# Kernel optimization log

Hardware: AMD Instinct MI355X
Metric: run time of the kernel (lower is better)

Reference implementation:

```python
import jax, jax.numpy as jnp
import numpy as np

D = 256
FF = 1024
NH = 8
BZ, TL = 8, 1024
L, Hs, Ws = 1, 64, 64


def _linear(x, w, b):
    # torch nn.Linear convention: w is [out, in]
    return x @ w.T + b


def _ln(x, g, b, eps=1e-5):
    m = x.mean(-1, keepdims=True)
    v = ((x - m) ** 2).mean(-1, keepdims=True)
    return (x - m) / jnp.sqrt(v + eps) * g + b


def setup_inputs() -> dict:
    key = jax.random.key(0)
    ks = jax.random.split(key, 16)
    s = 0.02
    inp = {
        "tgt": jax.random.normal(ks[0], (BZ, TL, D), jnp.float32),
        "reference_points": jax.random.uniform(ks[1], (BZ, TL, 2), jnp.float32),
        "srcs": jax.random.normal(ks[2], (BZ, L, D, Hs, Ws), jnp.float32),
        "posemb_2d": jax.random.normal(ks[3], (BZ, TL, D), jnp.float32),
        # self-attn (nn.MultiheadAttention) params
        "in_proj_w": jax.random.normal(ks[4], (3 * D, D), jnp.float32) * s,
        "in_proj_b": jnp.zeros((3 * D,), jnp.float32),
        "out_proj_w": jax.random.normal(ks[5], (D, D), jnp.float32) * s,
        "out_proj_b": jnp.zeros((D,), jnp.float32),
        # hand-rolled cross-attn linears (q, k, v, out)
        "lin_q_w": jax.random.normal(ks[6], (D, D), jnp.float32) * s,
        "lin_q_b": jnp.zeros((D,), jnp.float32),
        "lin_k_w": jax.random.normal(ks[7], (D, D), jnp.float32) * s,
        "lin_k_b": jnp.zeros((D,), jnp.float32),
        "lin_v_w": jax.random.normal(ks[8], (D, D), jnp.float32) * s,
        "lin_v_b": jnp.zeros((D,), jnp.float32),
        "lin_o_w": jax.random.normal(ks[9], (D, D), jnp.float32) * s,
        "lin_o_b": jnp.zeros((D,), jnp.float32),
        # layer norms
        "norm1_g": jnp.ones((D,), jnp.float32),
        "norm1_b": jnp.zeros((D,), jnp.float32),
        "norm2_g": jnp.ones((D,), jnp.float32),
        "norm2_b": jnp.zeros((D,), jnp.float32),
        # FFN
        "ffn_w1": jax.random.normal(ks[10], (FF, D), jnp.float32) * s,
        "ffn_b1": jnp.zeros((FF,), jnp.float32),
        "ffn_w2": jax.random.normal(ks[11], (D, FF), jnp.float32) * s,
        "ffn_b2": jnp.zeros((D,), jnp.float32),
        "ffn_norm_g": jnp.ones((D,), jnp.float32),
        "ffn_norm_b": jnp.zeros((D,), jnp.float32),
    }
    return inp


def reference(tgt, reference_points, srcs, posemb_2d,
              in_proj_w, in_proj_b, out_proj_w, out_proj_b,
              lin_q_w, lin_q_b, lin_k_w, lin_k_b, lin_v_w, lin_v_b,
              lin_o_w, lin_o_b,
              norm1_g, norm1_b, norm2_g, norm2_b,
              ffn_w1, ffn_b1, ffn_w2, ffn_b2, ffn_norm_g, ffn_norm_b):
    bz, tl, c = tgt.shape
    nh = NH
    dh = c // nh
    scale = dh ** -0.5

    # ---- self-attention (nn.MultiheadAttention math) ----
    qk = tgt + posemb_2d  # q = k = with_pos_embed(tgt, posemb_2d_)
    wq, wk, wv = in_proj_w[:c], in_proj_w[c:2 * c], in_proj_w[2 * c:]
    bq, bk, bv = in_proj_b[:c], in_proj_b[c:2 * c], in_proj_b[2 * c:]
    qp = _linear(qk, wq, bq).reshape(bz, tl, nh, dh)
    kp = _linear(qk, wk, bk).reshape(bz, tl, nh, dh)
    vp = _linear(tgt, wv, bv).reshape(bz, tl, nh, dh)
    att = jax.nn.softmax(jnp.einsum('bqhd,bkhd->bhqk', qp * scale, kp), axis=-1)
    sa = jnp.einsum('bhqk,bkhd->bqhd', att, vp).reshape(bz, tl, c)
    sa = _linear(sa, out_proj_w, out_proj_b)
    tgt = _ln(tgt + sa, norm2_g, norm2_b)

    # ---- hand-rolled cross attention ----
    bz_, l, c_, h, w = srcs.shape
    s = jnp.transpose(srcs.reshape(bz_ * l, c_, h, w), (0, 2, 3, 1)).reshape(bz_ * l, h * w, c_)
    query = _linear(tgt, lin_q_w, lin_q_b)          # [bz, tl, c]
    key = _linear(s, lin_k_w, lin_k_b)              # [bz*l, hw, c]
    value = _linear(s, lin_v_w, lin_v_b)
    affinity = jax.nn.softmax(jnp.einsum('bqc,bkc->bqk', query, key), axis=-1)  # no 1/sqrt(d) scale, faithful
    tgt2 = _linear(jnp.einsum('bqk,bkc->bqc', affinity, value), lin_o_w, lin_o_b)
    tgt = _ln(tgt + tgt2, norm1_g, norm1_b)

    # ---- FFN ----
    src2 = _linear(jax.nn.relu(_linear(tgt, ffn_w1, ffn_b1)), ffn_w2, ffn_b2)
    tgt = _ln(tgt + src2, ffn_norm_g, ffn_norm_b)
    return tgt
```

## Files before the change

### kernel.cpp

```cpp
#include <hip/hip_runtime.h>
#include <hip/hip_bf16.h>
#include <math.h>

typedef __attribute__((ext_vector_type(8))) __bf16 bf16x8;
typedef __attribute__((ext_vector_type(4))) __bf16 bf16x4;
typedef __attribute__((ext_vector_type(2))) __bf16 bf16x2;
typedef __attribute__((ext_vector_type(4))) float  f32x4;

#define MFMA16(a,b,c) __builtin_amdgcn_mfma_f32_16x16x32_bf16((a),(b),(c),0,0,0)

__device__ __forceinline__ unsigned pack2bf(float a, float b){
  bf16x2 t; t[0] = (__bf16)a; t[1] = (__bf16)b;
  return __builtin_bit_cast(unsigned, t);
}
__device__ __forceinline__ int perm1(int r){ return ((r<<2)|(r>>1)) & 7; }

__device__ __forceinline__ bf16x8 cvt8(const float4& a, const float4& b){
  bf16x8 h;
  h[0]=(__bf16)a.x; h[1]=(__bf16)a.y; h[2]=(__bf16)a.z; h[3]=(__bf16)a.w;
  h[4]=(__bf16)b.x; h[5]=(__bf16)b.y; h[6]=(__bf16)b.z; h[7]=(__bf16)b.w;
  return h;
}

template<int BM, bool RELU, int OUTMODE, int AMODE>
__global__ __launch_bounds__(256) void gemm_bt(
    const void* __restrict__ Av, const float* __restrict__ A2,
    const float* __restrict__ W,
    const float* __restrict__ bias, void* __restrict__ Cv,
    int M, int N, int K, int ldc, int coff, float oscale)
{
  constexpr int MT = BM/32;
  constexpr int PASSES = BM/64;
  __shared__ __align__(16) __bf16 As[BM][72];
  __shared__ __align__(16) __bf16 Bs[64][72];

  const int tid  = threadIdx.x;
  const int wid  = tid >> 6;
  const int lane = tid & 63;
  const int wr   = wid >> 1;
  const int wc   = wid & 1;
  const int lq   = lane & 15;
  const int lk8  = (lane >> 4) << 3;
  const int rb   = (lane >> 4) << 2;

  const int m0 = blockIdx.x * BM;
  const int n0 = blockIdx.y * 64;

  const int sr = tid >> 2;
  const int sc = (tid & 3) << 4;

  f32x4 acc[MT][2];
  #pragma unroll
  for (int i=0;i<MT;i++)
    #pragma unroll
    for (int j=0;j<2;j++) acc[i][j] = f32x4{0.f,0.f,0.f,0.f};

  for (int k0=0; k0<K; k0+=64){
    __syncthreads();
    #pragma unroll
    for (int p=0;p<PASSES;p++){
      const int row = sr + p*64;
      if (AMODE == 2){
        const __bf16* ap = (const __bf16*)Av + (size_t)(m0+row)*K + k0 + sc;
        *(bf16x8*)&As[row][sc]   = *(const bf16x8*)(ap);
        *(bf16x8*)&As[row][sc+8] = *(const bf16x8*)(ap + 8);
      } else {
        const float* ap = (const float*)Av + (size_t)(m0+row)*K + k0 + sc;
        float4 a0 = *(const float4*)(ap);
        float4 a1 = *(const float4*)(ap+4);
        float4 a2 = *(const float4*)(ap+8);
        float4 a3 = *(const float4*)(ap+12);
        if (AMODE == 1){
          const float* bp = A2 + (size_t)(m0+row)*K + k0 + sc;
          const float4 b0 = *(const float4*)(bp);
          const float4 b1 = *(const float4*)(bp+4);
          const float4 b2 = *(const float4*)(bp+8);
          const float4 b3 = *(const float4*)(bp+12);
          a0.x+=b0.x; a0.y+=b0.y; a0.z+=b0.z; a0.w+=b0.w;
          a1.x+=b1.x; a1.y+=b1.y; a1.z+=b1.z; a1.w+=b1.w;
          a2.x+=b2.x; a2.y+=b2.y; a2.z+=b2.z; a2.w+=b2.w;
          a3.x+=b3.x; a3.y+=b3.y; a3.z+=b3.z; a3.w+=b3.w;
        }
        *(bf16x8*)&As[row][sc]   = cvt8(a0,a1);
        *(bf16x8*)&As[row][sc+8] = cvt8(a2,a3);
      }
    }
    {
      const float* wp = W + (size_t)(n0+sr)*K + k0 + sc;
      const float4 a0 = *(const float4*)(wp);
      const float4 a1 = *(const float4*)(wp+4);
      const float4 a2 = *(const float4*)(wp+8);
      const float4 a3 = *(const float4*)(wp+12);
      *(bf16x8*)&Bs[sr][sc]   = cvt8(a0,a1);
      *(bf16x8*)&Bs[sr][sc+8] = cvt8(a2,a3);
    }
    __syncthreads();
    #pragma unroll
    for (int ksub=0; ksub<2; ksub++){
      bf16x8 bfr[2];
      #pragma unroll
      for (int j=0;j<2;j++)
        bfr[j] = *(const bf16x8*)&Bs[wc*32 + j*16 + lq][ksub*32 + lk8];
      #pragma unroll
      for (int i=0;i<MT;i++){
        const bf16x8 af = *(const bf16x8*)&As[wr*(BM/2) + i*16 + lq][ksub*32 + lk8];
        acc[i][0] = MFMA16(af, bfr[0], acc[i][0]);
        acc[i][1] = MFMA16(af, bfr[1], acc[i][1]);
      }
    }
  }

  #pragma unroll
  for (int i=0;i<MT;i++)
    #pragma unroll
    for (int j=0;j<2;j++){
      const int coln = n0 + wc*32 + j*16 + lq;
      const float bv = bias ? bias[coln] : 0.f;
      if (OUTMODE == 2){
        const int rowm0 = m0 + wr*(BM/2) + i*16 + rb;
        bf16x4 hv;
        #pragma unroll
        for (int r=0;r<4;r++){
          float vv = (acc[i][j][r] + bv) * oscale;
          if (RELU) vv = fmaxf(vv, 0.f);
          hv[r] = (__bf16)vv;
        }
        *(bf16x4*)&((__bf16*)Cv)[((size_t)((rowm0>>10)*256) + coln)*1024 + (rowm0&1023)] = hv;
      } else {
        #pragma unroll
        for (int r=0;r<4;r++){
          const int rowm = m0 + wr*(BM/2) + i*16 + rb + r;
          float vv = (acc[i][j][r] + bv) * oscale;
          if (RELU) vv = fmaxf(vv, 0.f);
          const size_t idx = (size_t)rowm*ldc + coff + coln;
          if (OUTMODE == 1) ((__bf16*)Cv)[idx] = (__bf16)vv;
          else              ((float*)Cv)[idx]  = vv;
        }
      }
    }
}

__global__ __launch_bounds__(256) void gemm_srcs_kv(
    const float* __restrict__ S,
    const float* __restrict__ Wk, const float* __restrict__ bk,
    const float* __restrict__ Wv, const float* __restrict__ bv,
    __bf16* __restrict__ Kout, __bf16* __restrict__ Vt)
{
  extern __shared__ __bf16 lds[];
  __bf16* As = lds;
  __bf16* Bs = lds + 128*264;

  const int tid  = threadIdx.x;
  const int wid  = tid >> 6;
  const int lane = tid & 63;
  const int wr   = wid >> 1;
  const int wc   = wid & 1;
  const int lq   = lane & 15;
  const int lk8  = (lane >> 4) << 3;
  const int rb   = (lane >> 4) << 2;

  const int m0 = blockIdx.x * 128;
  const int bb = m0 >> 12;
  const int p0 = m0 & 4095;

  const int cA = tid & 31;
  const int qA = tid >> 5;
  for (int k0=0; k0<256; k0+=32){
    const float* sbase = &S[((size_t)bb*256 + k0 + cA)*4096 + p0];
    #pragma unroll
    for (int ps=0; ps<4; ps++){
      const int p = ps*32 + qA*4;
      const float4 f4 = *(const float4*)(sbase + p);
      As[(p+0)*264 + k0 + cA] = (__bf16)f4.x;
      As[(p+1)*264 + k0 + cA] = (__bf16)f4.y;
      As[(p+2)*264 + k0 + cA] = (__bf16)f4.z;
      As[(p+3)*264 + k0 + cA] = (__bf16)f4.w;
    }
  }

  const int sr  = tid >> 2;
  const int scb = (tid & 3) * 64;

  for (int half=0; half<2; half++){
    const float* W    = half ? Wv : Wk;
    const float* bias = half ? bv : bk;
    for (int nt=0; nt<4; nt++){
      const int n0 = nt*64;
      __syncthreads();
      {
        const float* wp = W + (size_t)(n0+sr)*256 + scb;
        #pragma unroll
        for (int j=0;j<4;j++){
          const float4 a0 = *(const float4*)(wp + j*16);
          const float4 a1 = *(const float4*)(wp + j*16 + 4);
          const float4 a2 = *(const float4*)(wp + j*16 + 8);
          const float4 a3 = *(const float4*)(wp + j*16 + 12);
          *(bf16x8*)&Bs[sr*264 + scb + j*16]     = cvt8(a0,a1);
          *(bf16x8*)&Bs[sr*264 + scb + j*16 + 8] = cvt8(a2,a3);
        }
      }
      __syncthreads();
      f32x4 acc[4][2];
      #pragma unroll
      for (int i=0;i<4;i++)
        #pragma unroll
        for (int j=0;j<2;j++) acc[i][j] = f32x4{0.f,0.f,0.f,0.f};
      #pragma unroll
      for (int k0=0; k0<256; k0+=32){
        bf16x8 bfr[2];
        #pragma unroll
        for (int j=0;j<2;j++)
          bfr[j] = *(const bf16x8*)&Bs[(wc*32 + j*16 + lq)*264 + k0 + lk8];
        #pragma unroll
        for (int i=0;i<4;i++){
          const bf16x8 af = *(const bf16x8*)&As[(wr*64 + i*16 + lq)*264 + k0 + lk8];
          acc[i][0] = MFMA16(af, bfr[0], acc[i][0]);
          acc[i][1] = MFMA16(af, bfr[1], acc[i][1]);
        }
      }
      #pragma unroll
      for (int i=0;i<4;i++)
        #pragma unroll
        for (int j=0;j<2;j++){
          const int coln = n0 + wc*32 + j*16 + lq;
          const float bvv = bias[coln];
          if (half){
            bf16x4 hv;
            #pragma unroll
            for (int r=0;r<4;r++) hv[r] = (__bf16)(acc[i][j][r] + bvv);
            *(bf16x4*)&Vt[((size_t)bb*256 + coln)*4096 + p0 + wr*64 + i*16 + rb] = hv;
          } else {
            #pragma unroll
            for (int r=0;r<4;r++){
              const int rowm = m0 + wr*64 + i*16 + rb + r;
              Kout[(size_t)rowm*256 + coln] = (__bf16)(acc[i][j][r] + bvv);
            }
          }
        }
    }
  }
}

__global__ __launch_bounds__(256) void ln_kernel(const float* __restrict__ res,
                                                 const float* __restrict__ x,
                                                 const float* __restrict__ g,
                                                 const float* __restrict__ beta,
                                                 float* __restrict__ out,
                                                 __bf16* __restrict__ outb)
{
  const int row  = blockIdx.x*4 + (threadIdx.x >> 6);
  const int lane = threadIdx.x & 63;
  const int c = lane*4;
  const float4 rv = *(const float4*)&res[(size_t)row*256 + c];
  const float4 xv = *(const float4*)&x[(size_t)row*256 + c];
  float v0=rv.x+xv.x, v1=rv.y+xv.y, v2=rv.z+xv.z, v3=rv.w+xv.w;
  float s = v0+v1+v2+v3;
  #pragma unroll
  for (int off=1; off<64; off<<=1) s += __shfl_xor(s, off);
  const float mean = s * (1.f/256.f);
  const float d0=v0-mean, d1=v1-mean, d2=v2-mean, d3=v3-mean;
  float q = d0*d0 + d1*d1 + d2*d2 + d3*d3;
  #pragma unroll
  for (int off=1; off<64; off<<=1) q += __shfl_xor(q, off);
  const float rstd = rsqrtf(q*(1.f/256.f) + 1e-5f);
  const float4 gv = *(const float4*)&g[c];
  const float4 bv = *(const float4*)&beta[c];
  float4 ov;
  ov.x = d0*rstd*gv.x + bv.x;
  ov.y = d1*rstd*gv.y + bv.y;
  ov.z = d2*rstd*gv.z + bv.z;
  ov.w = d3*rstd*gv.w + bv.w;
  *(float4*)&out[(size_t)row*256 + c] = ov;
  if (outb){
    bf16x4 hv;
    hv[0]=(__bf16)ov.x; hv[1]=(__bf16)ov.y; hv[2]=(__bf16)ov.z; hv[3]=(__bf16)ov.w;
    *(bf16x4*)&outb[(size_t)row*256 + c] = hv;
  }
}

__global__ __launch_bounds__(256) void flash_self(
    const __bf16* __restrict__ qks, const __bf16* __restrict__ vts,
    __bf16* __restrict__ sab)
{
  const int qt = blockIdx.x;
  const int b  = blockIdx.y >> 3;
  const int h  = blockIdx.y & 7;
  const int tid  = threadIdx.x;
  const int wid  = tid >> 6;
  const int lane = tid & 63;
  const int lq   = lane & 15;
  const int hi   = lane >> 4;
  const int lk8  = hi << 3;
  const int rb   = hi << 2;
  const float SCALE = 0.17677669529663687f;

  const int qrow = b*1024 + qt*64 + wid*16 + lq;
  const bf16x8 qf = *(const bf16x8*)&qks[(size_t)qrow*512 + h*32 + lk8];

  const __bf16* kb0 = &qks[(size_t)(b*1024 + lq)*512 + 256 + h*32 + lk8];
  const __bf16* vb0 = &vts[(size_t)(b*256 + h*32 + lq)*1024 + lk8];

  const f32x4 Z = {0.f, 0.f, 0.f, 0.f};
  float m = -1e30f, l = 0.f;
  f32x4 o0 = Z, o1 = Z;

  for (int it=0; it<16; ++it){
    const int key0 = it*64;
    f32x4 s4[4];
    #pragma unroll
    for (int kt=0;kt<4;kt++){
      const bf16x8 kf = *(const bf16x8*)(kb0 + (size_t)(key0 + kt*16)*512);
      s4[kt] = MFMA16(kf, qf, Z);
      #pragma unroll
      for (int r=0;r<4;r++) s4[kt][r] *= SCALE;
    }
    float pm = s4[0][0];
    #pragma unroll
    for (int kt=0;kt<4;kt++)
      #pragma unroll
      for (int r=0;r<4;r++) pm = fmaxf(pm, s4[kt][r]);
    pm = fmaxf(pm, __shfl_xor(pm,16));
    pm = fmaxf(pm, __shfl_xor(pm,32));
    if (!__all(pm <= m + 8.f)){
      const float mn = fmaxf(m, pm);
      const float alpha = __expf(m - mn);
      o0[0]*=alpha; o0[1]*=alpha; o0[2]*=alpha; o0[3]*=alpha;
      o1[0]*=alpha; o1[1]*=alpha; o1[2]*=alpha; o1[3]*=alpha;
      l *= alpha;
      m = mn;
    }
    float p[4][4]; float rs = 0.f;
    #pragma unroll
    for (int kt=0;kt<4;kt++)
      #pragma unroll
      for (int r=0;r<4;r++){ p[kt][r] = __expf(s4[kt][r]-m); rs += p[kt][r]; }
    rs += __shfl_xor(rs,16);
    rs += __shfl_xor(rs,32);
    l += rs;
    unsigned pk0[4], pk1[4];
    #pragma unroll
    for (int kt=0;kt<4;kt++){
      pk0[kt] = pack2bf(p[kt][0], p[kt][1]);
      pk1[kt] = pack2bf(p[kt][2], p[kt][3]);
    }
    const int srcA = ((hi&1)<<5) + lq;
    const int srcB = srcA + 16;
    const bool ksel = hi >= 2;
    bf16x8 pf[2];
    #pragma unroll
    for (int ks2=0; ks2<2; ks2++){
      const unsigned a0 = (unsigned)__shfl((int)pk0[2*ks2],   srcA);
      const unsigned a1 = (unsigned)__shfl((int)pk0[2*ks2+1], srcA);
      const unsigned b0 = (unsigned)__shfl((int)pk1[2*ks2],   srcA);
      const unsigned b1 = (unsigned)__shfl((int)pk1[2*ks2+1], srcA);
      const unsigned c0 = (unsigned)__shfl((int)pk0[2*ks2],   srcB);
      const unsigned c1 = (unsigned)__shfl((int)pk0[2*ks2+1], srcB);
      const unsigned d0 = (unsigned)__shfl((int)pk1[2*ks2],   srcB);
      const unsigned d1 = (unsigned)__shfl((int)pk1[2*ks2+1], srcB);
      union { unsigned u[4]; bf16x8 v; } uu;
      uu.u[0] = ksel ? a1 : a0;
      uu.u[1] = ksel ? b1 : b0;
      uu.u[2] = ksel ? c1 : c0;
      uu.u[3] = ksel ? d1 : d0;
      pf[ks2] = uu.v;
    }
    #pragma unroll
    for (int ks2=0; ks2<2; ks2++){
      const bf16x8 vf0 = *(const bf16x8*)(vb0 + key0 + ks2*32);
      const bf16x8 vf1 = *(const bf16x8*)(vb0 + (size_t)16*1024 + key0 + ks2*32);
      o0 = MFMA16(vf0, pf[ks2], o0);
      o1 = MFMA16(vf1, pf[ks2], o1);
    }
  }
  const float inv = 1.f / l;
  bf16x4 w0, w1;
  #pragma unroll
  for (int r=0;r<4;r++){ w0[r] = (__bf16)(o0[r]*inv); w1[r] = (__bf16)(o1[r]*inv); }
  *(bf16x4*)&sab[(size_t)qrow*256 + h*32 + rb]      = w0;
  *(bf16x4*)&sab[(size_t)qrow*256 + h*32 + 16 + rb] = w1;
}

__global__ __launch_bounds__(256, 1) void flash_cross(
    const __bf16* __restrict__ qgm, const __bf16* __restrict__ kg,
    const __bf16* __restrict__ vtg, __bf16* __restrict__ Opart,
    float* __restrict__ ml)
{
  extern __shared__ __bf16 smem[];
  __bf16* Ks = smem;
  __bf16* Vt = smem + 64*256;

  const int bid = blockIdx.x;
  const int xcd = bid & 7;
  const int grp = bid >> 3;
  const int qt  = grp & 7;
  const int pp  = xcd + 8*(grp >> 3);
  const int b   = pp >> 3;
  const int sl  = pp & 7;

  const int tid  = threadIdx.x;
  const int wid  = tid >> 6;
  const int lane = tid & 63;
  const int lq   = lane & 15;
  const int hi   = lane >> 4;
  const int lk8  = hi << 3;
  const int rb   = hi << 2;
  const int p1l  = perm1(lq & 7);

  const int q0 = b*1024 + qt*128 + wid*32;
  bf16x8 qf[2][8];
  #pragma unroll
  for (int g=0; g<2; g++)
    #pragma unroll
    for (int ks=0; ks<8; ks++)
      qf[g][ks] = *(const bf16x8*)&qgm[(size_t)(q0 + g*16 + lq)*256 + ks*32 + lk8];

  const f32x4 Z = {0.f, 0.f, 0.f, 0.f};
  float m[2] = {-1e30f, -1e30f};
  float l[2] = {0.f, 0.f};
  f32x4 o[2][16];
  #pragma unroll
  for (int g=0; g<2; g++)
    #pragma unroll
    for (int nf=0; nf<16; nf++) o[g][nf] = Z;

  const int srow = tid >> 2;
  const int c4   = tid & 3;
  const int p1s  = perm1(srow & 7);

  for (int it=0; it<8; ++it){
    const int key0 = sl*512 + it*64;
    __syncthreads();
    {
      const __bf16* kb = &kg[(size_t)(b*4096 + key0 + srow)*256];
      #pragma unroll
      for (int j=0;j<8;j++){
        const int ch = c4 + j*4;
        *(bf16x8*)&Ks[srow*256 + ((ch ^ p1s)<<3)] = *(const bf16x8*)(kb + ch*8);
      }
    }
    {
      #pragma unroll
      for (int ps=0; ps<4; ps++){
        const int d = srow + ps*64;
        const __bf16* vb = &vtg[(size_t)(b*256 + d)*4096 + key0];
        #pragma unroll
        for (int s2=0;s2<2;s2++){
          const int ch = c4 + s2*4;
          *(bf16x8*)&Vt[d*64 + ((ch ^ p1s)<<3)] = *(const bf16x8*)(vb + ch*8);
        }
      }
    }
    __syncthreads();
    f32x4 s4[2][4];
    #pragma unroll
    for (int g=0; g<2; g++)
      #pragma unroll
      for (int kt=0;kt<4;kt++) s4[g][kt] = Z;
    #pragma unroll
    for (int ks=0; ks<8; ks++){
      #pragma unroll
      for (int kt=0; kt<4; kt++){
        const bf16x8 kf = *(const bf16x8*)&Ks[(kt*16+lq)*256 + (((ks*4+hi) ^ p1l)<<3)];
        s4[0][kt] = MFMA16(kf, qf[0][ks], s4[0][kt]);
        s4[1][kt] = MFMA16(kf, qf[1][ks], s4[1][kt]);
      }
    }
    float pm[2];
    #pragma unroll
    for (int g=0; g<2; g++){
      float v = s4[g][0][0];
      #pragma unroll
      for (int kt=0;kt<4;kt++)
        #pragma unroll
        for (int r=0;r<4;r++) v = fmaxf(v, s4[g][kt][r]);
      v = fmaxf(v, __shfl_xor(v, 16));
      v = fmaxf(v, __shfl_xor(v, 32));
      pm[g] = v;
    }
    const bool need = (pm[0] > m[0] + 8.f) || (pm[1] > m[1] + 8.f);
    if (__any(need)){
      #pragma unroll
      for (int g=0; g<2; g++){
        const float mn = fmaxf(m[g], pm[g]);
        const float alpha = __expf(m[g] - mn);
        #pragma unroll
        for (int nf=0;nf<16;nf++){
          o[g][nf][0]*=alpha; o[g][nf][1]*=alpha;
          o[g][nf][2]*=alpha; o[g][nf][3]*=alpha;
        }
        l[g] *= alpha;
        m[g] = mn;
      }
    }
    bf16x8 pf[2][2];
    #pragma unroll
    for (int g=0; g<2; g++){
      float p[4][4];
      float rs = 0.f;
      #pragma unroll
      for (int kt=0;kt<4;kt++)
        #pragma unroll
        for (int r=0;r<4;r++){ p[kt][r] = __expf(s4[g][kt][r] - m[g]); rs += p[kt][r]; }
      rs += __shfl_xor(rs, 16);
      rs += __shfl_xor(rs, 32);
      l[g] += rs;
      unsigned pk0[4], pk1[4];
      #pragma unroll
      for (int kt=0;kt<4;kt++){
        pk0[kt] = pack2bf(p[kt][0], p[kt][1]);
        pk1[kt] = pack2bf(p[kt][2], p[kt][3]);
      }
      const int srcA = ((hi&1)<<5) + lq;
      const int srcB = srcA + 16;
      const bool ksel = hi >= 2;
      #pragma unroll
      for (int ks2=0; ks2<2; ks2++){
        const unsigned a0 = (unsigned)__shfl((int)pk0[2*ks2],   srcA);
        const unsigned a1 = (unsigned)__shfl((int)pk0[2*ks2+1], srcA);
        const unsigned b0 = (unsigned)__shfl((int)pk1[2*ks2],   srcA);
        const unsigned b1 = (unsigned)__shfl((int)pk1[2*ks2+1], srcA);
        const unsigned c0 = (unsigned)__shfl((int)pk0[2*ks2],   srcB);
        const unsigned c1 = (unsigned)__shfl((int)pk0[2*ks2+1], srcB);
        const unsigned d0 = (unsigned)__shfl((int)pk1[2*ks2],   srcB);
        const unsigned d1 = (unsigned)__shfl((int)pk1[2*ks2+1], srcB);
        union { unsigned u[4]; bf16x8 v; } uu;
        uu.u[0] = ksel ? a1 : a0;
        uu.u[1] = ksel ? b1 : b0;
        uu.u[2] = ksel ? c1 : c0;
        uu.u[3] = ksel ? d1 : d0;
        pf[g][ks2] = uu.v;
      }
    }
    #pragma unroll
    for (int nf=0; nf<16; nf++){
      #pragma unroll
      for (int ks2=0; ks2<2; ks2++){
        const bf16x8 af = *(const bf16x8*)&Vt[(nf*16+lq)*64 + (((ks2*4+hi) ^ p1l)<<3)];
        o[0][nf] = MFMA16(af, pf[0][ks2], o[0][nf]);
        o[1][nf] = MFMA16(af, pf[1][ks2], o[1][nf]);
      }
    }
  }
  #pragma unroll
  for (int g=0; g<2; g++){
    const int row = q0 + g*16 + lq;
    if (hi == 0){
      ml[(size_t)(sl*8192 + row)*2 + 0] = m[g];
      ml[(size_t)(sl*8192 + row)*2 + 1] = l[g];
    }
    #pragma unroll
    for (int nf=0; nf<16; nf++){
      bf16x4 hv;
      #pragma unroll
      for (int r=0;r<4;r++) hv[r] = (__bf16)o[g][nf][r];
      *(bf16x4*)&Opart[(size_t)(sl*8192 + row)*256 + nf*16 + rb] = hv;
    }
  }
}

__global__ __launch_bounds__(256) void combine_kernel(const __bf16* __restrict__ Opart,
                                                      const float* __restrict__ ml,
                                                      __bf16* __restrict__ out)
{
  const int row = blockIdx.x;
  const int d = threadIdx.x;
  float mm[8], ll[8];
  #pragma unroll
  for (int s=0;s<8;s++){
    mm[s] = ml[(size_t)(s*8192+row)*2 + 0];
    ll[s] = ml[(size_t)(s*8192+row)*2 + 1];
  }
  float M = mm[0];
  #pragma unroll
  for (int s=1;s<8;s++) M = fmaxf(M, mm[s]);
  float L = 0.f, acc = 0.f;
  #pragma unroll
  for (int s=0;s<8;s++){
    const float e = __expf(mm[s]-M);
    L   += ll[s]*e;
    acc += e * (float)Opart[(size_t)(s*8192+row)*256 + d];
  }
  out[(size_t)row*256 + d] = (__bf16)(acc / L);
}

extern "C" void kernel_launch(void* const* d_in, const int* in_sizes, int n_in,
                              void* d_out, int out_size, void* d_ws, size_t ws_size,
                              hipStream_t stream)
{
  (void)in_sizes; (void)n_in; (void)out_size; (void)ws_size;
  const float* tgt        = (const float*)d_in[0];
  const float* srcs       = (const float*)d_in[2];
  const float* posemb     = (const float*)d_in[3];
  const float* in_proj_w  = (const float*)d_in[4];
  const float* in_proj_b  = (const float*)d_in[5];
  const float* out_proj_w = (const float*)d_in[6];
  const float* out_proj_b = (const float*)d_in[7];
  const float* lin_q_w    = (const float*)d_in[8];
  const float* lin_q_b    = (const float*)d_in[9];
  const float* lin_k_w    = (const float*)d_in[10];
  const float* lin_k_b    = (const float*)d_in[11];
  const float* lin_v_w    = (const float*)d_in[12];
  const float* lin_v_b    = (const float*)d_in[13];
  const float* lin_o_w    = (const float*)d_in[14];
  const float* lin_o_b    = (const float*)d_in[15];
  const float* norm1_g    = (const float*)d_in[16];
  const float* norm1_b    = (const float*)d_in[17];
  const float* norm2_g    = (const float*)d_in[18];
  const float* norm2_b    = (const float*)d_in[19];
  const float* ffn_w1     = (const float*)d_in[20];
  const float* ffn_b1     = (const float*)d_in[21];
  const float* ffn_w2     = (const float*)d_in[22];
  const float* ffn_b2     = (const float*)d_in[23];
  const float* ffn_norm_g = (const float*)d_in[24];
  const float* ffn_norm_b = (const float*)d_in[25];
  float* out = (float*)d_out;

  char* w = (char*)d_ws;
  const size_t MB = (size_t)1 << 20;
  float*  tgt1    = (float*)(w + 0);
  __bf16* qk_s    = (__bf16*)(w + 8*MB);
  __bf16* query_b = (__bf16*)(w + 8*MB);
  __bf16* tgt1b   = (__bf16*)(w + 12*MB);
  __bf16* attn2   = (__bf16*)(w + 12*MB);
  __bf16* v_t     = (__bf16*)(w + 16*MB);
  __bf16* key_b   = (__bf16*)(w + 16*MB);
  float*  t2proj  = (float*)(w + 16*MB);
  __bf16* sa_b    = (__bf16*)(w + 20*MB);
  float*  saproj  = (float*)(w + 24*MB);
  float*  tgt3    = (float*)(w + 24*MB);
  __bf16* val_t   = (__bf16*)(w + 32*MB);
  __bf16* ffn_h   = (__bf16*)(w + 32*MB);
  __bf16* Opart   = (__bf16*)(w + 48*MB);
  float*  ffn_out = (float*)(w + 48*MB);
  __bf16* tgt3b   = (__bf16*)(w + 56*MB);
  float*  ml      = (float*)(w + 80*MB);

  gemm_bt<64,false,1,1><<<dim3(128,8),256,0,stream>>>(tgt, posemb,
      in_proj_w, in_proj_b, qk_s, 8192,512,256, 512,0, 1.f);
  gemm_bt<64,false,2,0><<<dim3(128,4),256,0,stream>>>(tgt, nullptr,
      in_proj_w + 512*256, in_proj_b + 512, v_t, 8192,256,256, 256,0, 1.f);
  flash_self<<<dim3(16,64),256,0,stream>>>(qk_s, v_t, sa_b);
  gemm_bt<64,false,0,2><<<dim3(128,4),256,0,stream>>>(sa_b, nullptr,
      out_proj_w, out_proj_b, saproj, 8192,256,256, 256,0, 1.f);
  ln_kernel<<<2048,256,0,stream>>>(tgt, saproj, norm2_g, norm2_b, tgt1, tgt1b);

  gemm_bt<64,false,1,2><<<dim3(128,4),256,0,stream>>>(tgt1b, nullptr,
      lin_q_w, lin_q_b, query_b, 8192,256,256, 256,0, 1.f);
  gemm_srcs_kv<<<256,256,(128+64)*264*2,stream>>>(srcs,
      lin_k_w, lin_k_b, lin_v_w, lin_v_b, key_b, val_t);
  flash_cross<<<512,256,65536,stream>>>(query_b, key_b, val_t, Opart, ml);
  combine_kernel<<<8192,256,0,stream>>>(Opart, ml, attn2);
  gemm_bt<64,false,0,2><<<dim3(128,4),256,0,stream>>>(attn2, nullptr,
      lin_o_w, lin_o_b, t2proj, 8192,256,256, 256,0, 1.f);
  ln_kernel<<<2048,256,0,stream>>>(tgt1, t2proj, norm1_g, norm1_b, tgt3, tgt3b);

  gemm_bt<128,true,1,2><<<dim3(64,16),256,0,stream>>>(tgt3b, nullptr,
      ffn_w1, ffn_b1, ffn_h, 8192,1024,256, 1024,0, 1.f);
  gemm_bt<64,false,0,2><<<dim3(128,4),256,0,stream>>>(ffn_h, nullptr,
      ffn_w2, ffn_b2, ffn_out, 8192,256,1024, 256,0, 1.f);
  ln_kernel<<<2048,256,0,stream>>>(tgt3, ffn_out, ffn_norm_g, ffn_norm_b, out, nullptr);
}
```

Baseline: 286.5 us.

## Fuse output-projection GEMMs with residual add and LayerNorm

```diff
diff --git a/kernel.cpp b/kernel.cpp
--- a/kernel.cpp
+++ b/kernel.cpp
@@ -140,6 +140,134 @@
     }
 }
 
+template<int BM, int NW>
+__global__ __launch_bounds__(NW*64) void gemm_ln(
+    const __bf16* __restrict__ A, const float* __restrict__ W,
+    const float* __restrict__ bias, const float* __restrict__ res,
+    const float* __restrict__ g, const float* __restrict__ beta,
+    float* __restrict__ out, __bf16* __restrict__ outb, int K)
+{
+  constexpr int NTH = NW*64;
+  constexpr int CW  = 256/NW;
+  constexpr int MT  = BM/16;
+  constexpr int NT  = CW/16;
+  __shared__ __align__(16) __bf16 As[BM][72];
+  __shared__ __align__(16) __bf16 Bs[256][72];
+  __shared__ float red_s[NW][BM];
+  __shared__ float red_q[NW][BM];
+
+  const int tid  = threadIdx.x;
+  const int w    = tid >> 6;
+  const int lane = tid & 63;
+  const int lq   = lane & 15;
+  const int hi   = lane >> 4;
+  const int lk8  = hi << 3;
+  const int rb   = hi << 2;
+
+  const int m0 = blockIdx.x * BM;
+
+  f32x4 acc[MT][NT];
+  #pragma unroll
+  for (int i=0;i<MT;i++)
+    #pragma unroll
+    for (int j=0;j<NT;j++) acc[i][j] = f32x4{0.f,0.f,0.f,0.f};
+
+  constexpr int BROWS = NTH/4;
+  const int sr = tid >> 2;
+  const int sc = (tid & 3) << 4;
+
+  for (int k0=0; k0<K; k0+=64){
+    __syncthreads();
+    if (tid < BM*8){
+      const int row = tid >> 3;
+      const int c8  = (tid & 7) << 3;
+      *(bf16x8*)&As[row][c8] =
+        *(const bf16x8*)((const __bf16*)A + (size_t)(m0+row)*K + k0 + c8);
+    }
+    #pragma unroll
+    for (int p=0; p<256/BROWS; p++){
+      const int row = p*BROWS + sr;
+      const float* wp = W + (size_t)row*K + k0 + sc;
+      const float4 a0 = *(const float4*)(wp);
+      const float4 a1 = *(const float4*)(wp+4);
+      const float4 a2 = *(const float4*)(wp+8);
+      const float4 a3 = *(const float4*)(wp+12);
+      *(bf16x8*)&Bs[row][sc]   = cvt8(a0,a1);
+      *(bf16x8*)&Bs[row][sc+8] = cvt8(a2,a3);
+    }
+    __syncthreads();
+    #pragma unroll
+    for (int ksub=0; ksub<2; ksub++){
+      bf16x8 af[MT];
+      #pragma unroll
+      for (int i=0;i<MT;i++)
+        af[i] = *(const bf16x8*)&As[i*16 + lq][ksub*32 + lk8];
+      #pragma unroll
+      for (int j=0;j<NT;j++){
+        const bf16x8 bfr = *(const bf16x8*)&Bs[w*CW + j*16 + lq][ksub*32 + lk8];
+        #pragma unroll
+        for (int i=0;i<MT;i++)
+          acc[i][j] = MFMA16(af[i], bfr, acc[i][j]);
+      }
+    }
+  }
+
+  float vals[MT][NT][4];
+  #pragma unroll
+  for (int i=0;i<MT;i++)
+    #pragma unroll
+    for (int j=0;j<NT;j++){
+      const int coln = w*CW + j*16 + lq;
+      const float bv = bias[coln];
+      #pragma unroll
+      for (int r=0;r<4;r++){
+        const int rowm = m0 + i*16 + rb + r;
+        vals[i][j][r] = acc[i][j][r] + bv + res[(size_t)rowm*256 + coln];
+      }
+    }
+  #pragma unroll
+  for (int i=0;i<MT;i++){
+    #pragma unroll
+    for (int r=0;r<4;r++){
+      float s = 0.f, q = 0.f;
+      #pragma unroll
+      for (int j=0;j<NT;j++){ const float v = vals[i][j][r]; s += v; q += v*v; }
+      #pragma unroll
+      for (int off=1; off<16; off<<=1){
+        s += __shfl_xor(s, off);
+        q += __shfl_xor(q, off);
+      }
+      if (lq == 0){
+        const int rl = i*16 + rb + r;
+        red_s[w][rl] = s;
+        red_q[w][rl] = q;
+      }
+    }
+  }
+  __syncthreads();
+  #pragma unroll
+  for (int i=0;i<MT;i++){
+    #pragma unroll
+    for (int r=0;r<4;r++){
+      const int rl = i*16 + rb + r;
+      float s = 0.f, q = 0.f;
+      #pragma unroll
+      for (int ww=0; ww<NW; ww++){ s += red_s[ww][rl]; q += red_q[ww][rl]; }
+      const float mean = s * (1.f/256.f);
+      const float var  = q * (1.f/256.f) - mean*mean;
+      const float rstd = rsqrtf(var + 1e-5f);
+      const int rowm = m0 + rl;
+      #pragma unroll
+      for (int j=0;j<NT;j++){
+        const int coln = w*CW + j*16 + lq;
+        const float ov = (vals[i][j][r] - mean) * rstd * g[coln] + beta[coln];
+        out[(size_t)rowm*256 + coln] = ov;
+        if (outb) outb[(size_t)rowm*256 + coln] = (__bf16)ov;
+      }
+    }
+  }
+}
+
 __global__ __launch_bounds__(256) void gemm_srcs_kv(
     const float* __restrict__ S,
     const float* __restrict__ Wk, const float* __restrict__ bk,
@@ -238,43 +366,6 @@
           }
         }
     }
-  }
-}
-
-__global__ __launch_bounds__(256) void ln_kernel(const float* __restrict__ res,
-                                                 const float* __restrict__ x,
-                                                 const float* __restrict__ g,
-                                                 const float* __restrict__ beta,
-                                                 float* __restrict__ out,
-                                                 __bf16* __restrict__ outb)
-{
-  const int row  = blockIdx.x*4 + (threadIdx.x >> 6);
-  const int lane = threadIdx.x & 63;
-  const int c = lane*4;
-  const float4 rv = *(const float4*)&res[(size_t)row*256 + c];
-  const float4 xv = *(const float4*)&x[(size_t)row*256 + c];
-  float v0=rv.x+xv.x, v1=rv.y+xv.y, v2=rv.z+xv.z, v3=rv.w+xv.w;
-  float s = v0+v1+v2+v3;
-  #pragma unroll
-  for (int off=1; off<64; off<<=1) s += __shfl_xor(s, off);
-  const float mean = s * (1.f/256.f);
-  const float d0=v0-mean, d1=v1-mean, d2=v2-mean, d3=v3-mean;
-  float q = d0*d0 + d1*d1 + d2*d2 + d3*d3;
-  #pragma unroll
-  for (int off=1; off<64; off<<=1) q += __shfl_xor(q, off);
-  const float rstd = rsqrtf(q*(1.f/256.f) + 1e-5f);
-  const float4 gv = *(const float4*)&g[c];
-  const float4 bv = *(const float4*)&beta[c];
-  float4 ov;
-  ov.x = d0*rstd*gv.x + bv.x;
-  ov.y = d1*rstd*gv.y + bv.y;
-  ov.z = d2*rstd*gv.z + bv.z;
-  ov.w = d3*rstd*gv.w + bv.w;
-  *(float4*)&out[(size_t)row*256 + c] = ov;
-  if (outb){
-    bf16x4 hv;
-    hv[0]=(__bf16)ov.x; hv[1]=(__bf16)ov.y; hv[2]=(__bf16)ov.z; hv[3]=(__bf16)ov.w;
-    *(bf16x4*)&outb[(size_t)row*256 + c] = hv;
   }
 }
 
@@ -624,14 +715,11 @@
   __bf16* attn2   = (__bf16*)(w + 12*MB);
   __bf16* v_t     = (__bf16*)(w + 16*MB);
   __bf16* key_b   = (__bf16*)(w + 16*MB);
-  float*  t2proj  = (float*)(w + 16*MB);
   __bf16* sa_b    = (__bf16*)(w + 20*MB);
-  float*  saproj  = (float*)(w + 24*MB);
   float*  tgt3    = (float*)(w + 24*MB);
   __bf16* val_t   = (__bf16*)(w + 32*MB);
   __bf16* ffn_h   = (__bf16*)(w + 32*MB);
   __bf16* Opart   = (__bf16*)(w + 48*MB);
-  float*  ffn_out = (float*)(w + 48*MB);
   __bf16* tgt3b   = (__bf16*)(w + 56*MB);
   float*  ml      = (float*)(w + 80*MB);
 
@@ -640,9 +728,8 @@
   gemm_bt<64,false,2,0><<<dim3(128,4),256,0,stream>>>(tgt, nullptr,
       in_proj_w + 512*256, in_proj_b + 512, v_t, 8192,256,256, 256,0, 1.f);
   flash_self<<<dim3(16,64),256,0,stream>>>(qk_s, v_t, sa_b);
-  gemm_bt<64,false,0,2><<<dim3(128,4),256,0,stream>>>(sa_b, nullptr,
-      out_proj_w, out_proj_b, saproj, 8192,256,256, 256,0, 1.f);
-  ln_kernel<<<2048,256,0,stream>>>(tgt, saproj, norm2_g, norm2_b, tgt1, tgt1b);
+  gemm_ln<16,4><<<512,256,0,stream>>>(sa_b, out_proj_w, out_proj_b,
+      tgt, norm2_g, norm2_b, tgt1, tgt1b, 256);
 
   gemm_bt<64,false,1,2><<<dim3(128,4),256,0,stream>>>(tgt1b, nullptr,
       lin_q_w, lin_q_b, query_b, 8192,256,256, 256,0, 1.f);
@@ -650,13 +737,11 @@
       lin_k_w, lin_k_b, lin_v_w, lin_v_b, key_b, val_t);
   flash_cross<<<512,256,65536,stream>>>(query_b, key_b, val_t, Opart, ml);
   combine_kernel<<<8192,256,0,stream>>>(Opart, ml, attn2);
-  gemm_bt<64,false,0,2><<<dim3(128,4),256,0,stream>>>(attn2, nullptr,
-      lin_o_w, lin_o_b, t2proj, 8192,256,256, 256,0, 1.f);
-  ln_kernel<<<2048,256,0,stream>>>(tgt1, t2proj, norm1_g, norm1_b, tgt3, tgt3b);
+  gemm_ln<16,4><<<512,256,0,stream>>>(attn2, lin_o_w, lin_o_b,
+      tgt1, norm1_g, norm1_b, tgt3, tgt3b, 256);
 
   gemm_bt<128,true,1,2><<<dim3(64,16),256,0,stream>>>(tgt3b, nullptr,
       ffn_w1, ffn_b1, ffn_h, 8192,1024,256, 1024,0, 1.f);
-  gemm_bt<64,false,0,2><<<dim3(128,4),256,0,stream>>>(ffn_h, nullptr,
-      ffn_w2, ffn_b2, ffn_out, 8192,256,1024, 256,0, 1.f);
-  ln_kernel<<<2048,256,0,stream>>>(tgt3, ffn_out, ffn_norm_g, ffn_norm_b, out, nullptr);
-}
+  gemm_ln<32,8><<<256,512,0,stream>>>(ffn_h, ffn_w2, ffn_b2,
+      tgt3, ffn_norm_g, ffn_norm_b, out, nullptr, 1024);
+}
```

New measurement: 292.3 us. 1.02x slower.
